# Kernel optimization log

Hardware: AMD Instinct MI355X
Metric: run time of the kernel (lower is better)

The kernel has to match this reference:

```python
import jax, jax.numpy as jnp
import numpy as np

L, B, D = 4096, 4, 512  # seq_len, batch, embed_dim (nhead=1 so kdim=vdim=D)


def setup_inputs() -> dict:
    key = jax.random.key(0)
    ks = jax.random.split(key, 11)
    sc = 1.0 / np.sqrt(D)
    return {
        "x": jax.random.normal(ks[0], (L, B, D), jnp.float32),
        "e": jax.random.normal(ks[1], (L, B, D), jnp.float32),
        "relay": jax.random.normal(ks[2], (1, B, D), jnp.float32),
        "Wq": jax.random.normal(ks[3], (D, D), jnp.float32) * sc,
        "bq": jax.random.normal(ks[4], (D,), jnp.float32) * sc,
        "Wk": jax.random.normal(ks[5], (D, D), jnp.float32) * sc,
        "bk": jax.random.normal(ks[6], (D,), jnp.float32) * sc,
        "Wv": jax.random.normal(ks[7], (D, D), jnp.float32) * sc,
        "bv": jax.random.normal(ks[8], (D,), jnp.float32) * sc,
        "Wo": jax.random.normal(ks[9], (D, D), jnp.float32) * sc,
        "bo": jax.random.normal(ks[10], (D,), jnp.float32) * sc,
    }


def _window3(t):
    # t: [L,B,D] -> [L,B,3,D] with zero padding at the sequence boundaries
    # (matches nn.Unfold(kernel=[3,1], padding=[1,0]): positions l-1, l, l+1)
    n = t.shape[0]
    tp = jnp.pad(t, ((1, 1), (0, 0), (0, 0)))
    return jnp.stack([tp[:n], tp[1:n + 1], tp[2:n + 2]], axis=2)


def reference(x, e, relay, Wq, bq, Wk, bk, Wv, bv, Wo, bo):
    l, b, d = x.shape
    scale = 1.0 / jnp.sqrt(jnp.asarray(d, x.dtype))

    q = x @ Wq.T + bq          # [L,B,D]
    k = x @ Wk.T + bk
    v = x @ Wv.T + bv

    # cores = [embedding tokens e ; relay broadcast over L]  -> [2,L,B,D]
    s = jnp.broadcast_to(relay, (l, b, d))
    cores = jnp.stack([e, s], axis=0)
    k_c = cores @ Wk.T + bk    # [2,L,B,D]
    v_c = cores @ Wv.T + bv

    # ring (local windowed) attention: window = [k_{l-1},k_l,k_{l+1}, k(e_l), k(relay)]
    kw = jnp.concatenate([_window3(k), jnp.transpose(k_c, (1, 2, 0, 3))], axis=2)  # [L,B,5,D]
    vw = jnp.concatenate([_window3(v), jnp.transpose(v_c, (1, 2, 0, 3))], axis=2)  # [L,B,5,D]
    logits = jnp.einsum('lbd,lbwd->lbw', q, kw) * scale
    alphas = jax.nn.softmax(logits, axis=2)
    ring = jnp.einsum('lbw,lbwd->lbd', alphas, vw)  # [L,B,D]

    # star (relay) attention: query is the UNprojected relay token (as in source)
    k_r = relay @ Wk.T + bk    # [1,B,D]
    v_r = relay @ Wv.T + bv
    kk = jnp.concatenate([k, k_r], axis=0)  # [L+1,B,D]
    vv = jnp.concatenate([v, v_r], axis=0)
    s_logits = jnp.einsum('obd,nbd->bon', relay, kk) * scale  # [B,1,L+1]
    s_alphas = jax.nn.softmax(s_logits, axis=-1)
    star = jnp.einsum('bon,nbd->obd', s_alphas, vv)  # [1,B,D]

    return (ring @ Wo.T + bo, star @ Wo.T + bo)
```

## Files before the change

### kernel.cpp

```cpp
#include <hip/hip_runtime.h>
#include <hip/hip_fp16.h>

#define L_SEQ 4096
#define BATCH 4
#define DIM 512
#define M_ROWS (L_SEQ * BATCH)
#define SCALE 0.04419417382415922f
#define SLS 4097

typedef __attribute__((ext_vector_type(4))) float f32x4;
typedef __attribute__((ext_vector_type(8))) _Float16 f16x8;
typedef __attribute__((ext_vector_type(4))) _Float16 f16x4;

__device__ inline void gload16(const void* g, void* l) {
    __builtin_amdgcn_global_load_lds(
        (const __attribute__((address_space(1))) void*)g,
        (__attribute__((address_space(3))) void*)l, 16, 0, 0);
}

__device__ inline float wred_sum(float s) {
#pragma unroll
    for (int o = 32; o; o >>= 1) s += __shfl_xor(s, o);
    return s;
}
__device__ inline float wred_max(float s) {
#pragma unroll
    for (int o = 32; o; o >>= 1) s = fmaxf(s, __shfl_xor(s, o));
    return s;
}

__global__ __launch_bounds__(256) void prep(
    const float* __restrict__ x, const float* __restrict__ e,
    const float* __restrict__ Wq, const float* __restrict__ Wk,
    const float* __restrict__ Wv, const float* __restrict__ Wo,
    const float* __restrict__ bq, const float* __restrict__ bk, const float* __restrict__ bv,
    _Float16* __restrict__ xh, _Float16* __restrict__ eh,
    _Float16* __restrict__ Wqkv, _Float16* __restrict__ Wof, float* __restrict__ bqkv)
{
    const int bid = blockIdx.x;
    if (bid < 16384) {
        size_t i = (size_t)bid * 256 + threadIdx.x;
        const size_t NV = (size_t)M_ROWS * DIM / 4;
        const float* src; _Float16* dst; size_t j;
        if (i < NV) { src = x; dst = xh; j = i; } else { src = e; dst = eh; j = i - NV; }
        float4 v = ((const float4*)src)[j];
        f16x4 h = { (_Float16)v.x, (_Float16)v.y, (_Float16)v.z, (_Float16)v.w };
        ((f16x4*)dst)[j] = h;
    } else {
        int i = (bid - 16384) * 256 + threadIdx.x;
        {
            int r = i >> 9, c = i & 511;
            const float* W = (r < 512) ? Wq : (r < 1024 ? Wk : Wv);
            Wqkv[i] = (_Float16)W[(size_t)(r & 511) * 512 + c];
        }
        if (i < 512 * 512) Wof[i] = (_Float16)Wo[i];
        if (i < 1536) bqkv[i] = (i < 512) ? bq[i] : (i < 1024 ? bk[i - 512] : bv[i - 1024]);
    }
}

__global__ __launch_bounds__(256) void relay_proj(
    const float* __restrict__ relay,
    const float* __restrict__ Wk, const float* __restrict__ bk,
    const float* __restrict__ Wv, const float* __restrict__ bv,
    float* __restrict__ krvr, float* __restrict__ star)
{
    const int o = (blockIdx.x << 2) + (threadIdx.x >> 6);
    const int lane = threadIdx.x & 63;
    const int sel = o >> 11, rem = o & 2047, b = rem >> 9, j = rem & 511;
    const float* W = sel ? Wv : Wk;
    const float* wr = W + (size_t)j * 512 + lane * 8;
    const float* rp = relay + (size_t)b * 512 + lane * 8;
    float4 w0 = *(const float4*)wr,  w1 = *(const float4*)(wr + 4);
    float4 r0 = *(const float4*)rp,  r1 = *(const float4*)(rp + 4);
    float s = w0.x * r0.x + w0.y * r0.y + w0.z * r0.z + w0.w * r0.w
            + w1.x * r1.x + w1.y * r1.y + w1.z * r1.z + w1.w * r1.w;
    s = wred_sum(s);
    if (lane == 0) {
        krvr[o] = s + (sel ? bv[j] : bk[j]);
        if (o < 2048) star[o] = 0.f;
    }
}

template<int OUT16>
__global__ __launch_bounds__(256) void gemm_bt(
    const _Float16* __restrict__ A, const _Float16* __restrict__ Bm,
    const float* __restrict__ bias, void* __restrict__ Cv,
    int M, int N, int K)
{
    __shared__ _Float16 lA[128 * 32];
    __shared__ _Float16 lB[128 * 32];
    const int tid = threadIdx.x;
    const int wave = tid >> 6, lane = tid & 63;
    const int row0 = blockIdx.x * 128;
    const int col0 = blockIdx.y * 128;
    const int wm = (wave >> 1) * 64, wn = (wave & 1) * 64;

    f32x4 acc[4][4];
#pragma unroll
    for (int i = 0; i < 4; ++i)
#pragma unroll
        for (int j = 0; j < 4; ++j) acc[i][j] = (f32x4)0.f;

    const int c0 = wave * 64 + lane;
    const int c1 = 256 + c0;
    const int ar0 = c0 >> 2, ac0 = (c0 & 3) * 8;
    const int ar1 = c1 >> 2, ac1 = (c1 & 3) * 8;
    _Float16* dstA0 = lA + (wave * 64) * 8;
    _Float16* dstA1 = lA + (256 + wave * 64) * 8;
    _Float16* dstB0 = lB + (wave * 64) * 8;
    _Float16* dstB1 = lB + (256 + wave * 64) * 8;

    const int nsteps = K >> 5;
    auto stage = [&](int k0) {
        gload16(A  + (size_t)(row0 + ar0) * K + k0 + ac0, dstA0);
        gload16(A  + (size_t)(row0 + ar1) * K + k0 + ac1, dstA1);
        gload16(Bm + (size_t)(col0 + ar0) * K + k0 + ac0, dstB0);
        gload16(Bm + (size_t)(col0 + ar1) * K + k0 + ac1, dstB1);
    };
    stage(0);

    for (int t = 0; t < nsteps; ++t) {
        __syncthreads();
        const int aro = (wm + (lane & 15)) * 32 + (lane >> 4) * 8;
        const int bro = (wn + (lane & 15)) * 32 + (lane >> 4) * 8;
        f16x8 af[4], bfr[4];
#pragma unroll
        for (int i = 0; i < 4; ++i) af[i]  = *(const f16x8*)(lA + aro + i * 16 * 32);
#pragma unroll
        for (int i = 0; i < 4; ++i) bfr[i] = *(const f16x8*)(lB + bro + i * 16 * 32);
        __syncthreads();
        if (t + 1 < nsteps) stage((t + 1) << 5);
#pragma unroll
        for (int mi = 0; mi < 4; ++mi)
#pragma unroll
            for (int ni = 0; ni < 4; ++ni)
                acc[mi][ni] = __builtin_amdgcn_mfma_f32_16x16x32_f16(
                    af[mi], bfr[ni], acc[mi][ni], 0, 0, 0);
    }

#pragma unroll
    for (int mi = 0; mi < 4; ++mi) {
#pragma unroll
        for (int ni = 0; ni < 4; ++ni) {
            const int col = col0 + wn + ni * 16 + (lane & 15);
            const float bb = bias[col];
#pragma unroll
            for (int r = 0; r < 4; ++r) {
                const int row = row0 + wm + mi * 16 + (lane >> 4) * 4 + r;
                float v = acc[mi][ni][r] + bb;
                if (OUT16) ((_Float16*)Cv)[(size_t)row * N + col] = (_Float16)v;
                else       ((float*)Cv)[(size_t)row * N + col] = v;
            }
        }
    }
}

__global__ __launch_bounds__(256) void ring_attn(
    const _Float16* __restrict__ qkv,
    const _Float16* __restrict__ ekv,
    const float* __restrict__ krvr,
    const float* __restrict__ relay,
    _Float16* __restrict__ ring,
    float* __restrict__ slog)
{
    const int wid = (blockIdx.x << 2) + (threadIdx.x >> 6);
    const int lane = threadIdx.x & 63;
    const int r = wid, b = r & 3, l = r >> 2;
    const int d0 = lane << 3;

    float q[8], rl[8];
    {
        f16x8 t = *(const f16x8*)(qkv + (size_t)r * 1536 + d0);
#pragma unroll
        for (int i = 0; i < 8; ++i) q[i] = (float)t[i];
        const float* rp = relay + (size_t)b * 512 + d0;
        float4 a = *(const float4*)rp, c = *(const float4*)(rp + 4);
        rl[0] = a.x; rl[1] = a.y; rl[2] = a.z; rl[3] = a.w;
        rl[4] = c.x; rl[5] = c.y; rl[6] = c.z; rl[7] = c.w;
    }
    const bool has0 = (l > 0), has2 = (l < L_SEQ - 1);

    auto dotk = [&](const _Float16* kp) -> float {
        f16x8 t = *(const f16x8*)(kp + d0);
        float s = 0.f;
#pragma unroll
        for (int i = 0; i < 8; ++i) s += q[i] * (float)t[i];
        return wred_sum(s);
    };

    float lg[5];
    lg[0] = has0 ? dotk(qkv + (size_t)(r - 4) * 1536 + 512) : 0.f;
    lg[2] = has2 ? dotk(qkv + (size_t)(r + 4) * 1536 + 512) : 0.f;
    lg[3] = dotk(ekv + (size_t)r * 1024);
    {
        f16x8 t = *(const f16x8*)(qkv + (size_t)r * 1536 + 512 + d0);
        float s1 = 0.f, s2 = 0.f;
#pragma unroll
        for (int i = 0; i < 8; ++i) { float kf = (float)t[i]; s1 += q[i] * kf; s2 += rl[i] * kf; }
#pragma unroll
        for (int o = 32; o; o >>= 1) { s1 += __shfl_xor(s1, o); s2 += __shfl_xor(s2, o); }
        lg[1] = s1;
        if (lane == 0) slog[(size_t)b * SLS + l] = s2 * SCALE;
    }
    {
        const float* kp = krvr + (size_t)b * 512 + d0;
        float s = 0.f;
#pragma unroll
        for (int i = 0; i < 8; ++i) s += q[i] * kp[i];
        lg[4] = wred_sum(s);
    }

    float li[5], m = -1e30f;
#pragma unroll
    for (int w = 0; w < 5; ++w) { li[w] = lg[w] * SCALE; m = fmaxf(m, li[w]); }
    float ew[5], Z = 0.f;
#pragma unroll
    for (int w = 0; w < 5; ++w) { ew[w] = expf(li[w] - m); Z += ew[w]; }
    const float inv = 1.f / Z;

    float o8[8] = {0, 0, 0, 0, 0, 0, 0, 0};
    auto addv = [&](const _Float16* vp, float a) {
        f16x8 t = *(const f16x8*)(vp + d0);
#pragma unroll
        for (int i = 0; i < 8; ++i) o8[i] += a * (float)t[i];
    };
    if (has0) addv(qkv + (size_t)(r - 4) * 1536 + 1024, ew[0] * inv);
    addv(qkv + (size_t)r * 1536 + 1024, ew[1] * inv);
    if (has2) addv(qkv + (size_t)(r + 4) * 1536 + 1024, ew[2] * inv);
    addv(ekv + (size_t)r * 1024 + 512, ew[3] * inv);
    {
        const float* vp = krvr + 2048 + (size_t)b * 512 + d0;
        const float a = ew[4] * inv;
#pragma unroll
        for (int i = 0; i < 8; ++i) o8[i] += a * vp[i];
    }
    f16x8 res;
#pragma unroll
    for (int i = 0; i < 8; ++i) res[i] = (_Float16)o8[i];
    *(f16x8*)(ring + (size_t)r * 512 + d0) = res;
}

__global__ __launch_bounds__(1024) void star_softmax(
    const float* __restrict__ relay, const float* __restrict__ krvr,
    float* __restrict__ slog)
{
    const int b = blockIdx.x, t = threadIdx.x, lane = t & 63, w = t >> 6;
    __shared__ float red[16];
    __shared__ float bc[2];
    float* sl = slog + (size_t)b * SLS;

    float p = 0.f;
    if (t < 512) p = relay[(size_t)b * 512 + t] * krvr[(size_t)b * 512 + t];
    p = wred_sum(p);
    if (lane == 0) red[w] = p;
    __syncthreads();
    if (t == 0) { float s = 0.f; for (int i = 0; i < 16; ++i) s += red[i]; bc[0] = s * SCALE; }
    __syncthreads();
    const float selfl = bc[0];
    __syncthreads();

    float v[4];
#pragma unroll
    for (int i = 0; i < 4; ++i) v[i] = sl[t + i * 1024];

    float m = selfl;
#pragma unroll
    for (int i = 0; i < 4; ++i) m = fmaxf(m, v[i]);
    m = wred_max(m);
    if (lane == 0) red[w] = m;
    __syncthreads();
    if (t == 0) { float mm = red[0]; for (int i = 1; i < 16; ++i) mm = fmaxf(mm, red[i]); bc[1] = mm; }
    __syncthreads();
    m = bc[1];

    float ev[4], z = (t == 0) ? expf(selfl - m) : 0.f;
#pragma unroll
    for (int i = 0; i < 4; ++i) { ev[i] = expf(v[i] - m); z += ev[i]; }
    z = wred_sum(z);
    if (lane == 0) red[w] = z;
    __syncthreads();
    if (t == 0) { float s = 0.f; for (int i = 0; i < 16; ++i) s += red[i]; bc[0] = 1.f / s; }
    __syncthreads();
    const float inv = bc[0];

#pragma unroll
    for (int i = 0; i < 4; ++i) sl[t + i * 1024] = ev[i] * inv;
    if (t == 0) sl[SLS - 1] = expf(selfl - m) * inv;
}

__global__ __launch_bounds__(256) void star_out(
    const float* __restrict__ slog, const _Float16* __restrict__ qkv,
    const float* __restrict__ krvr, float* __restrict__ star)
{
    const int b = threadIdx.x >> 6, lane = threadIdx.x & 63;
    const int chunk = blockIdx.x;
    const int d0 = lane << 3;
    const float* al = slog + (size_t)b * SLS;
    float acc[8] = {0, 0, 0, 0, 0, 0, 0, 0};
#pragma unroll 4
    for (int i = 0; i < 64; ++i) {
        const int n = chunk * 64 + i;
        const float a = al[n];
        f16x8 v = *(const f16x8*)(qkv + (size_t)(n * 4 + b) * 1536 + 1024 + d0);
#pragma unroll
        for (int j = 0; j < 8; ++j) acc[j] += a * (float)v[j];
    }
    if (chunk == 63) {
        const float a = al[SLS - 1];
        const float* vr = krvr + 2048 + (size_t)b * 512 + d0;
#pragma unroll
        for (int j = 0; j < 8; ++j) acc[j] += a * vr[j];
    }
#pragma unroll
    for (int j = 0; j < 8; ++j) atomicAdd(&star[(size_t)b * 512 + d0 + j], acc[j]);
}

__global__ __launch_bounds__(256) void star_proj(
    const float* __restrict__ star, const float* __restrict__ Wo,
    const float* __restrict__ bo, float* __restrict__ out1)
{
    const int o = (blockIdx.x << 2) + (threadIdx.x >> 6);
    const int lane = threadIdx.x & 63;
    const int b = o >> 9, j = o & 511;
    const float* sp = star + (size_t)b * 512 + lane * 8;
    const float* wr = Wo + (size_t)j * 512 + lane * 8;
    float4 w0 = *(const float4*)wr,  w1 = *(const float4*)(wr + 4);
    float4 s0 = *(const float4*)sp,  s1 = *(const float4*)(sp + 4);
    float s = w0.x * s0.x + w0.y * s0.y + w0.z * s0.z + w0.w * s0.w
            + w1.x * s1.x + w1.y * s1.y + w1.z * s1.z + w1.w * s1.w;
    s = wred_sum(s);
    if (lane == 0) out1[o] = s + bo[j];
}

extern "C" void kernel_launch(void* const* d_in, const int* in_sizes, int n_in,
                              void* d_out, int out_size, void* d_ws, size_t ws_size,
                              hipStream_t stream) {
    const float* x     = (const float*)d_in[0];
    const float* e     = (const float*)d_in[1];
    const float* relay = (const float*)d_in[2];
    const float* Wq    = (const float*)d_in[3];
    const float* bq    = (const float*)d_in[4];
    const float* Wk    = (const float*)d_in[5];
    const float* bk    = (const float*)d_in[6];
    const float* Wv    = (const float*)d_in[7];
    const float* bv    = (const float*)d_in[8];
    const float* Wo    = (const float*)d_in[9];
    const float* bo    = (const float*)d_in[10];
    float* out = (float*)d_out;

    size_t off = 0;
    auto alloc = [&](size_t bytes) {
        void* p = (char*)d_ws + off;
        off += (bytes + 255) & ~(size_t)255;
        return p;
    };
    _Float16* Wqkv = (_Float16*)alloc((size_t)1536 * 512 * 2);
    _Float16* Wof  = (_Float16*)alloc((size_t)512 * 512 * 2);
    float*    bqkv = (float*)   alloc(1536 * 4);
    _Float16* xh   = (_Float16*)alloc((size_t)M_ROWS * 512 * 2);
    _Float16* eh   = (_Float16*)alloc((size_t)M_ROWS * 512 * 2);
    _Float16* qkv  = (_Float16*)alloc((size_t)M_ROWS * 1536 * 2);
    _Float16* ekv  = (_Float16*)alloc((size_t)M_ROWS * 1024 * 2);
    float*    krvr = (float*)   alloc(2 * 4 * 512 * 4);
    float*    slog = (float*)   alloc((size_t)4 * SLS * 4);
    float*    star = (float*)   alloc(4 * 512 * 4);
    _Float16* ringb = xh;

    prep<<<16384 + 3072, 256, 0, stream>>>(x, e, Wq, Wk, Wv, Wo, bq, bk, bv,
                                           xh, eh, Wqkv, Wof, bqkv);
    relay_proj<<<1024, 256, 0, stream>>>(relay, Wk, bk, Wv, bv, krvr, star);

    gemm_bt<1><<<dim3(M_ROWS / 128, 1536 / 128), 256, 0, stream>>>(
        xh, Wqkv, bqkv, qkv, M_ROWS, 1536, 512);
    gemm_bt<1><<<dim3(M_ROWS / 128, 1024 / 128), 256, 0, stream>>>(
        eh, Wqkv + (size_t)512 * 512, bqkv + 512, ekv, M_ROWS, 1024, 512);

    ring_attn<<<M_ROWS / 4, 256, 0, stream>>>(qkv, ekv, krvr, relay, ringb, slog);

    star_softmax<<<4, 1024, 0, stream>>>(relay, krvr, slog);
    star_out<<<64, 256, 0, stream>>>(slog, qkv, krvr, star);

    gemm_bt<0><<<dim3(M_ROWS / 128, 512 / 128), 256, 0, stream>>>(
        ringb, Wof, bo, out, M_ROWS, 512, 512);
    star_proj<<<512, 256, 0, stream>>>(star, Wo, bo, out + (size_t)M_ROWS * 512);
}
```

Baseline: 160.7 us.

## Double-buffer GEMM LDS with swizzle and fold relay projection into prep

The GEMM main loop now uses two LDS buffers, prefetching two k-steps ahead. Explicit vmcnt/lgkmcnt waits and a single barrier per phase replace the two __syncthreads, so global-to-LDS loads overlap the MFMA work. LDS columns are XOR-swizzled to reduce bank conflicts, and MFMA issue is wrapped in s_setprio. Separately, the relay projection kernel is merged into the prep launch to save one kernel launch, at the cost of doubled LDS per block and correctness that depends on the hand-counted vmcnt values.

Result: no change. 160.8 us (+0.1%).

```diff
diff --git a/kernel.cpp b/kernel.cpp
--- a/kernel.cpp
+++ b/kernel.cpp
@@ -34,8 +34,10 @@
     const float* __restrict__ Wq, const float* __restrict__ Wk,
     const float* __restrict__ Wv, const float* __restrict__ Wo,
     const float* __restrict__ bq, const float* __restrict__ bk, const float* __restrict__ bv,
+    const float* __restrict__ relay,
     _Float16* __restrict__ xh, _Float16* __restrict__ eh,
-    _Float16* __restrict__ Wqkv, _Float16* __restrict__ Wof, float* __restrict__ bqkv)
+    _Float16* __restrict__ Wqkv, _Float16* __restrict__ Wof, float* __restrict__ bqkv,
+    float* __restrict__ krvr, float* __restrict__ star)
 {
     const int bid = blockIdx.x;
     if (bid < 16384) {
@@ -46,7 +48,7 @@
         float4 v = ((const float4*)src)[j];
         f16x4 h = { (_Float16)v.x, (_Float16)v.y, (_Float16)v.z, (_Float16)v.w };
         ((f16x4*)dst)[j] = h;
-    } else {
+    } else if (bid < 19456) {
         int i = (bid - 16384) * 256 + threadIdx.x;
         {
             int r = i >> 9, c = i & 511;
@@ -55,29 +57,22 @@
         }
         if (i < 512 * 512) Wof[i] = (_Float16)Wo[i];
         if (i < 1536) bqkv[i] = (i < 512) ? bq[i] : (i < 1024 ? bk[i - 512] : bv[i - 1024]);
-    }
-}
-
-__global__ __launch_bounds__(256) void relay_proj(
-    const float* __restrict__ relay,
-    const float* __restrict__ Wk, const float* __restrict__ bk,
-    const float* __restrict__ Wv, const float* __restrict__ bv,
-    float* __restrict__ krvr, float* __restrict__ star)
-{
-    const int o = (blockIdx.x << 2) + (threadIdx.x >> 6);
-    const int lane = threadIdx.x & 63;
-    const int sel = o >> 11, rem = o & 2047, b = rem >> 9, j = rem & 511;
-    const float* W = sel ? Wv : Wk;
-    const float* wr = W + (size_t)j * 512 + lane * 8;
-    const float* rp = relay + (size_t)b * 512 + lane * 8;
-    float4 w0 = *(const float4*)wr,  w1 = *(const float4*)(wr + 4);
-    float4 r0 = *(const float4*)rp,  r1 = *(const float4*)(rp + 4);
-    float s = w0.x * r0.x + w0.y * r0.y + w0.z * r0.z + w0.w * r0.w
-            + w1.x * r1.x + w1.y * r1.y + w1.z * r1.z + w1.w * r1.w;
-    s = wred_sum(s);
-    if (lane == 0) {
-        krvr[o] = s + (sel ? bv[j] : bk[j]);
-        if (o < 2048) star[o] = 0.f;
+    } else {
+        const int o = ((bid - 19456) << 2) + (threadIdx.x >> 6);
+        const int lane = threadIdx.x & 63;
+        const int sel = o >> 11, rem = o & 2047, b = rem >> 9, j = rem & 511;
+        const float* W = sel ? Wv : Wk;
+        const float* wr = W + (size_t)j * 512 + lane * 8;
+        const float* rp = relay + (size_t)b * 512 + lane * 8;
+        float4 w0 = *(const float4*)wr,  w1 = *(const float4*)(wr + 4);
+        float4 r0 = *(const float4*)rp,  r1 = *(const float4*)(rp + 4);
+        float s = w0.x * r0.x + w0.y * r0.y + w0.z * r0.z + w0.w * r0.w
+                + w1.x * r1.x + w1.y * r1.y + w1.z * r1.z + w1.w * r1.w;
+        s = wred_sum(s);
+        if (lane == 0) {
+            krvr[o] = s + (sel ? bv[j] : bk[j]);
+            if (o < 2048) star[o] = 0.f;
+        }
     }
 }
 
@@ -87,8 +82,8 @@
     const float* __restrict__ bias, void* __restrict__ Cv,
     int M, int N, int K)
 {
-    __shared__ _Float16 lA[128 * 32];
-    __shared__ _Float16 lB[128 * 32];
+    __shared__ _Float16 lA[2][128 * 32];
+    __shared__ _Float16 lB[2][128 * 32];
     const int tid = threadIdx.x;
     const int wave = tid >> 6, lane = tid & 63;
     const int row0 = blockIdx.x * 128;
@@ -101,41 +96,49 @@
 #pragma unroll
         for (int j = 0; j < 4; ++j) acc[i][j] = (f32x4)0.f;
 
-    const int c0 = wave * 64 + lane;
-    const int c1 = 256 + c0;
-    const int ar0 = c0 >> 2, ac0 = (c0 & 3) * 8;
-    const int ar1 = c1 >> 2, ac1 = (c1 & 3) * 8;
-    _Float16* dstA0 = lA + (wave * 64) * 8;
-    _Float16* dstA1 = lA + (256 + wave * 64) * 8;
-    _Float16* dstB0 = lB + (wave * 64) * 8;
-    _Float16* dstB1 = lB + (256 + wave * 64) * 8;
+    const int idx0 = tid, idx1 = 256 + tid;
+    const int r0_ = idx0 >> 2, c0_ = ((idx0 & 3) ^ ((idx0 >> 3) & 3)) * 8;
+    const int r1_ = idx1 >> 2, c1_ = ((idx1 & 3) ^ ((idx1 >> 3) & 3)) * 8;
+    const int ldsb0 = (wave * 64) * 8;
+    const int ldsb1 = (256 + wave * 64) * 8;
 
     const int nsteps = K >> 5;
-    auto stage = [&](int k0) {
-        gload16(A  + (size_t)(row0 + ar0) * K + k0 + ac0, dstA0);
-        gload16(A  + (size_t)(row0 + ar1) * K + k0 + ac1, dstA1);
-        gload16(Bm + (size_t)(col0 + ar0) * K + k0 + ac0, dstB0);
-        gload16(Bm + (size_t)(col0 + ar1) * K + k0 + ac1, dstB1);
+    auto stage = [&](int buf, int t) {
+        const int k0 = t << 5;
+        gload16(A  + (size_t)(row0 + r0_) * K + k0 + c0_, &lA[buf][ldsb0]);
+        gload16(A  + (size_t)(row0 + r1_) * K + k0 + c1_, &lA[buf][ldsb1]);
+        gload16(Bm + (size_t)(col0 + r0_) * K + k0 + c0_, &lB[buf][ldsb0]);
+        gload16(Bm + (size_t)(col0 + r1_) * K + k0 + c1_, &lB[buf][ldsb1]);
     };
-    stage(0);
-
+    stage(0, 0);
+    stage(1, 1);
+
+    const int rslot = ((lane >> 4) ^ ((lane >> 1) & 3)) * 8;
+    const int arb = (wm + (lane & 15)) * 32 + rslot;
+    const int brb = (wn + (lane & 15)) * 32 + rslot;
+
+    int cur = 0;
     for (int t = 0; t < nsteps; ++t) {
-        __syncthreads();
-        const int aro = (wm + (lane & 15)) * 32 + (lane >> 4) * 8;
-        const int bro = (wn + (lane & 15)) * 32 + (lane >> 4) * 8;
+        if (t + 1 < nsteps) asm volatile("s_waitcnt vmcnt(4)" ::: "memory");
+        else                asm volatile("s_waitcnt vmcnt(0)" ::: "memory");
+        __builtin_amdgcn_s_barrier();
         f16x8 af[4], bfr[4];
 #pragma unroll
-        for (int i = 0; i < 4; ++i) af[i]  = *(const f16x8*)(lA + aro + i * 16 * 32);
-#pragma unroll
-        for (int i = 0; i < 4; ++i) bfr[i] = *(const f16x8*)(lB + bro + i * 16 * 32);
-        __syncthreads();
-        if (t + 1 < nsteps) stage((t + 1) << 5);
+        for (int i = 0; i < 4; ++i) af[i]  = *(const f16x8*)(&lA[cur][arb + i * 512]);
+#pragma unroll
+        for (int i = 0; i < 4; ++i) bfr[i] = *(const f16x8*)(&lB[cur][brb + i * 512]);
+        __builtin_amdgcn_s_setprio(1);
 #pragma unroll
         for (int mi = 0; mi < 4; ++mi)
 #pragma unroll
             for (int ni = 0; ni < 4; ++ni)
                 acc[mi][ni] = __builtin_amdgcn_mfma_f32_16x16x32_f16(
                     af[mi], bfr[ni], acc[mi][ni], 0, 0, 0);
+        __builtin_amdgcn_s_setprio(0);
+        asm volatile("s_waitcnt lgkmcnt(0)" ::: "memory");
+        __builtin_amdgcn_s_barrier();
+        if (t + 2 < nsteps) stage(cur, t + 2);
+        cur ^= 1;
     }
 
 #pragma unroll
@@ -366,9 +369,9 @@
     float*    star = (float*)   alloc(4 * 512 * 4);
     _Float16* ringb = xh;
 
-    prep<<<16384 + 3072, 256, 0, stream>>>(x, e, Wq, Wk, Wv, Wo, bq, bk, bv,
-                                           xh, eh, Wqkv, Wof, bqkv);
-    relay_proj<<<1024, 256, 0, stream>>>(relay, Wk, bk, Wv, bv, krvr, star);
+    prep<<<16384 + 3072 + 1024, 256, 0, stream>>>(
+        x, e, Wq, Wk, Wv, Wo, bq, bk, bv, relay,
+        xh, eh, Wqkv, Wof, bqkv, krvr, star);
 
     gemm_bt<1><<<dim3(M_ROWS / 128, 1536 / 128), 256, 0, stream>>>(
         xh, Wqkv, bqkv, qkv, M_ROWS, 1536, 512);
```
